# Optimization experiments

Measured on AMD Instinct MI355X. Metric: run time of the kernel, lower is better.

## Reference

```python
import jax, jax.numpy as jnp
import numpy as np

D_MODEL = 1024
NUM_HEADS = 16
D_HEAD = D_MODEL // NUM_HEADS
BATCH = 2
SEQ = 2048


def setup_inputs() -> dict:
    key = jax.random.key(0)
    ks = jax.random.split(key, 5)
    std = 0.02
    return {
        "x": jax.random.normal(ks[0], (BATCH, SEQ, D_MODEL), dtype=jnp.float32),
        "Wq": jax.random.normal(ks[1], (D_MODEL, D_MODEL), dtype=jnp.float32) * std,
        "Wk": jax.random.normal(ks[2], (D_MODEL, D_MODEL), dtype=jnp.float32) * std,
        "Wv": jax.random.normal(ks[3], (D_MODEL, D_MODEL), dtype=jnp.float32) * std,
        "Wo": jax.random.normal(ks[4], (D_MODEL, D_MODEL), dtype=jnp.float32) * std,
    }


def reference(x, Wq, Wk, Wv, Wo):
    batch, seq_len, d_model = x.shape
    h, dh = NUM_HEADS, D_HEAD

    def split_heads(W):
        # x @ W.T -> (b, s, d) -> (b, h, s, dh)
        p = jnp.einsum('bsd,ed->bse', x, W)
        return p.reshape(batch, seq_len, h, dh).transpose(0, 2, 1, 3)

    Q = split_heads(Wq)
    K = split_heads(Wk)
    V = split_heads(Wv)

    scale = 1.0 / jnp.sqrt(jnp.asarray(dh, dtype=x.dtype))
    scores = jnp.einsum('bhqd,bhkd->bhqk', Q, K) * scale
    causal = jnp.tril(jnp.ones((seq_len, seq_len), dtype=bool))
    scores = jnp.where(causal, scores, -jnp.inf)
    attn = jax.nn.softmax(scores, axis=-1)
    out = jnp.einsum('bhqk,bhkd->bhqd', attn, V)  # (b, h, s, dh)
    out = out.transpose(0, 2, 1, 3).reshape(batch, seq_len, d_model)
    return jnp.einsum('bsd,ed->bse', out, Wo)
```

## Files before the change

kernel.cpp:

```cpp
#include <hip/hip_runtime.h>

#define D_MODEL 1024
#define NUM_HEADS 16
#define D_HEAD 64
#define BATCH 2
#define SEQ 2048
#define MTOT (BATCH * SEQ)
#define PLANE ((size_t)MTOT * D_MODEL)
#define QSCALE 0.1803368801f

typedef unsigned short us;
typedef __bf16 bf16x8 __attribute__((ext_vector_type(8)));
typedef float floatx4 __attribute__((ext_vector_type(4)));

__device__ __forceinline__ unsigned int f2bf(float f) {
  union { float f; unsigned int i; } v; v.f = f;
  unsigned int r = v.i + 0x7FFFu + ((v.i >> 16) & 1u);
  return r >> 16;
}
__device__ __forceinline__ unsigned int f2bf_tr(float f) {
  union { float f; unsigned int i; } v; v.f = f;
  return v.i >> 16;
}

__global__ __launch_bounds__(256) void convert_all(const float* __restrict__ x,
                                                   const float* __restrict__ Wq,
                                                   const float* __restrict__ Wk,
                                                   const float* __restrict__ Wv,
                                                   const float* __restrict__ Wo,
                                                   us* __restrict__ xbf,
                                                   us* __restrict__ Wqkv,
                                                   us* __restrict__ Wobf) {
  const int i = blockIdx.x * 256 + threadIdx.x;
  const float* src;
  us* dst;
  if (i < (1 << 20)) {
    src = x + (size_t)i * 4;
    dst = xbf + (size_t)i * 4;
  } else {
    const int j = i - (1 << 20);
    const int w = j >> 18;
    const int o = j & ((1 << 18) - 1);
    if (w < 3) {
      const float* ws = (w == 0) ? Wq : (w == 1) ? Wk : Wv;
      src = ws + (size_t)o * 4;
      dst = Wqkv + (size_t)w * (D_MODEL * D_MODEL) + (size_t)o * 4;
    } else {
      src = Wo + (size_t)o * 4;
      dst = Wobf + (size_t)o * 4;
    }
  }
  float4 v = *(const float4*)src;
  uint2 pk;
  pk.x = f2bf(v.x) | (f2bf(v.y) << 16);
  pk.y = f2bf(v.z) | (f2bf(v.w) << 16);
  *(uint2*)dst = pk;
}

template <int CMODE>
__global__ __launch_bounds__(256) void gemm_mfma(const us* __restrict__ A,
                                                 const us* __restrict__ B,
                                                 void* __restrict__ Cv,
                                                 int M, int N, int K) {
  __shared__ __bf16 As[2][128 * 32];
  __shared__ __bf16 Bs[2][128 * 32];
  const int tid = threadIdx.x;
  const int wid = tid >> 6;
  const int lane = tid & 63;
  const int bm = blockIdx.y * 128;
  const int bn = blockIdx.x * 128;
  const int wm = (wid & 1) * 64;
  const int wn = (wid >> 1) * 64;
  const int lr = lane & 15;
  const int quad = lane >> 4;

  floatx4 acc[4][4] = {};
  const int cb0 = wid * 128;

  auto stage = [&](int buf, int k0) {
#pragma unroll
    for (int p = 0; p < 2; ++p) {
      const int cb = cb0 + p * 64;
      const int c = cb + lane;
      const us* ga = A + (size_t)(bm + (c >> 2)) * K + (k0 + (c & 3) * 8);
      const us* gb = B + (size_t)(bn + (c >> 2)) * K + (k0 + (c & 3) * 8);
      __builtin_amdgcn_global_load_lds((const __attribute__((address_space(1))) void*)ga,
                                       (__attribute__((address_space(3))) void*)(&As[buf][cb * 8]),
                                       16, 0, 0);
      __builtin_amdgcn_global_load_lds((const __attribute__((address_space(1))) void*)gb,
                                       (__attribute__((address_space(3))) void*)(&Bs[buf][cb * 8]),
                                       16, 0, 0);
    }
  };

  stage(0, 0);
  __syncthreads();

  int cur = 0;
  for (int k0 = 0; k0 < K; k0 += 32) {
    if (k0 + 32 < K) stage(cur ^ 1, k0 + 32);

    bf16x8 a[4], b[4];
#pragma unroll
    for (int i = 0; i < 4; ++i)
      a[i] = *(const bf16x8*)&As[cur][(wm + i * 16 + lr) * 32 + quad * 8];
#pragma unroll
    for (int j = 0; j < 4; ++j)
      b[j] = *(const bf16x8*)&Bs[cur][(wn + j * 16 + lr) * 32 + quad * 8];
#pragma unroll
    for (int i = 0; i < 4; ++i)
#pragma unroll
      for (int j = 0; j < 4; ++j)
        acc[i][j] = __builtin_amdgcn_mfma_f32_16x16x32_bf16(a[i], b[j], acc[i][j], 0, 0, 0);

    __syncthreads();
    cur ^= 1;
  }

#pragma unroll
  for (int i = 0; i < 4; ++i) {
#pragma unroll
    for (int j = 0; j < 4; ++j) {
      const int col = bn + wn + j * 16 + lr;
      if constexpr (CMODE == 1) {
        us* dst = (us*)Cv;
        const int plane = col >> 10;
        if (plane < 2) {
          const float s = (plane == 0) ? QSCALE : 1.0f;
#pragma unroll
          for (int r = 0; r < 4; ++r) {
            const int row = bm + wm + i * 16 + quad * 4 + r;
            dst[(size_t)plane * PLANE + (size_t)row * 1024 + (col & 1023)] =
                (us)f2bf(acc[i][j][r] * s);
          }
        } else {
          const int d = col & 63;
          const int hh = (col >> 6) & 15;
          const int row0 = bm + wm + i * 16 + quad * 4;
          const int bb = row0 >> 11;
          const int ss = row0 & 2047;
          uint2 pk;
          pk.x = f2bf(acc[i][j][0]) | (f2bf(acc[i][j][1]) << 16);
          pk.y = f2bf(acc[i][j][2]) | (f2bf(acc[i][j][3]) << 16);
          *(uint2*)&dst[2 * PLANE + ((size_t)((bb * 16 + hh) * 64 + d)) * 2048 + ss] = pk;
        }
      } else {
#pragma unroll
        for (int r = 0; r < 4; ++r) {
          const int row = bm + wm + i * 16 + quad * 4 + r;
          ((float*)Cv)[(size_t)row * N + col] = acc[i][j][r];
        }
      }
    }
  }
}

__global__ __launch_bounds__(256) void gemm_n64(const us* __restrict__ A,
                                                const us* __restrict__ B,
                                                float* __restrict__ C,
                                                int M, int N, int K) {
  __shared__ __bf16 As[2][128 * 32];
  __shared__ __bf16 Bs[2][64 * 32];
  const int tid = threadIdx.x;
  const int wid = tid >> 6;
  const int lane = tid & 63;
  const int bm = blockIdx.y * 128;
  const int bn = blockIdx.x * 64;
  const int wm = wid * 32;
  const int lr = lane & 15;
  const int quad = lane >> 4;

  floatx4 acc[2][4] = {};

  auto stage = [&](int buf, int k0) {
#pragma unroll
    for (int p = 0; p < 2; ++p) {
      const int cb = wid * 128 + p * 64;
      const int c = cb + lane;
      const us* ga = A + (size_t)(bm + (c >> 2)) * K + (k0 + (c & 3) * 8);
      __builtin_amdgcn_global_load_lds((const __attribute__((address_space(1))) void*)ga,
                                       (__attribute__((address_space(3))) void*)(&As[buf][cb * 8]),
                                       16, 0, 0);
    }
    const int cb2 = wid * 64;
    const int c2 = cb2 + lane;
    const us* gb = B + (size_t)(bn + (c2 >> 2)) * K + (k0 + (c2 & 3) * 8);
    __builtin_amdgcn_global_load_lds((const __attribute__((address_space(1))) void*)gb,
                                     (__attribute__((address_space(3))) void*)(&Bs[buf][cb2 * 8]),
                                     16, 0, 0);
  };

  stage(0, 0);
  __syncthreads();

  int cur = 0;
  for (int k0 = 0; k0 < K; k0 += 32) {
    if (k0 + 32 < K) stage(cur ^ 1, k0 + 32);

    bf16x8 a[2], b[4];
#pragma unroll
    for (int i = 0; i < 2; ++i)
      a[i] = *(const bf16x8*)&As[cur][(wm + i * 16 + lr) * 32 + quad * 8];
#pragma unroll
    for (int j = 0; j < 4; ++j)
      b[j] = *(const bf16x8*)&Bs[cur][(j * 16 + lr) * 32 + quad * 8];
#pragma unroll
    for (int i = 0; i < 2; ++i)
#pragma unroll
      for (int j = 0; j < 4; ++j)
        acc[i][j] = __builtin_amdgcn_mfma_f32_16x16x32_bf16(a[i], b[j], acc[i][j], 0, 0, 0);

    __syncthreads();
    cur ^= 1;
  }

#pragma unroll
  for (int i = 0; i < 2; ++i) {
#pragma unroll
    for (int j = 0; j < 4; ++j) {
      const int col = bn + j * 16 + lr;
#pragma unroll
      for (int r = 0; r < 4; ++r) {
        const int row = bm + wm + i * 16 + quad * 4 + r;
        C[(size_t)row * N + col] = acc[i][j][r];
      }
    }
  }
}

#define ASTR 72

__global__ __launch_bounds__(512, 2) void attn_mfma(const us* __restrict__ Qb,
                                                    const us* __restrict__ Kb,
                                                    const us* __restrict__ Vtg,
                                                    us* __restrict__ Ob) {
  const int bx = blockIdx.x;
  const int b = bx >> 8;
  const int idx = bx & 255;
  const int h = idx >> 4;
  const int s0 = idx & 15;
  const int strip = b ? (15 - s0) : s0;
  const int q0 = strip * 128;
  const int ntiles = 2 * strip + 2;
  const int tid = threadIdx.x;
  const int w = tid >> 6;
  const int lane = tid & 63;
  const int lr = lane & 15;
  const int quad = lane >> 4;

  __shared__ us Ks[2][64 * ASTR];
  __shared__ us Vs[2][64 * ASTR];
  __shared__ us Ps[8 * 16 * ASTR];

  const us* kbase = Kb + (size_t)(b * SEQ) * D_MODEL + h * D_HEAD;
  const us* vbase = Vtg + (size_t)((b * 16 + h) * 64) * 2048;
  us* const pg = &Ps[w * 16 * ASTR];

  const int grow = q0 + w * 16;
  const us* qp = Qb + (size_t)(b * SEQ + grow + lr) * D_MODEL + h * D_HEAD;
  const bf16x8 qa0 = *(const bf16x8*)(qp + quad * 8);
  const bf16x8 qa1 = *(const bf16x8*)(qp + 32 + quad * 8);

  floatx4 oacc[4] = {};
  floatx4 lacc = {};
  bf16x8 ones;
#pragma unroll
  for (int i = 0; i < 8; ++i) ones[i] = (__bf16)1.0f;

  const int srow = tid >> 3;
  const int schunk = tid & 7;

  uint4 kreg, vreg;
  kreg = *(const uint4*)(kbase + (size_t)srow * D_MODEL + schunk * 8);
  vreg = *(const uint4*)(vbase + (size_t)srow * 2048 + schunk * 8);
  *(uint4*)&Ks[0][srow * ASTR + schunk * 8] = kreg;
  *(uint4*)&Vs[0][srow * ASTR + schunk * 8] = vreg;
  __syncthreads();

  for (int t = 0; t < ntiles; ++t) {
    const int k0 = t * 64;
    const int cur = t & 1;
    const bool more = (t + 1 < ntiles);

    if (more) {
      const int kn = k0 + 64;
      kreg = *(const uint4*)(kbase + (size_t)(kn + srow) * D_MODEL + schunk * 8);
      vreg = *(const uint4*)(vbase + (size_t)srow * 2048 + kn + schunk * 8);
    }

#pragma unroll
    for (int jt = 0; jt < 4; ++jt) {
      const bf16x8 kb0 = *(const bf16x8*)&Ks[cur][(jt * 16 + lr) * ASTR + quad * 8];
      const bf16x8 kb1 = *(const bf16x8*)&Ks[cur][(jt * 16 + lr) * ASTR + 32 + quad * 8];
      floatx4 s = {};
      s = __builtin_amdgcn_mfma_f32_16x16x32_bf16(kb0, qa0, s, 0, 0, 0);
      s = __builtin_amdgcn_mfma_f32_16x16x32_bf16(kb1, qa1, s, 0, 0, 0);
      const int kb = k0 + jt * 16 + quad * 4;
      const bool needMask = (k0 + jt * 16 + 15 > grow);
      float p[4];
#pragma unroll
      for (int r = 0; r < 4; ++r) {
        float e = __builtin_amdgcn_exp2f(s[r]);
        if (needMask && (kb + r > grow + lr)) e = 0.f;
        p[r] = e;
      }
      uint2 pk;
      pk.x = f2bf_tr(p[0]) | (f2bf_tr(p[1]) << 16);
      pk.y = f2bf_tr(p[2]) | (f2bf_tr(p[3]) << 16);
      *(uint2*)&pg[lr * ASTR + jt * 16 + quad * 4] = pk;
    }

    const bf16x8 pa0 = *(const bf16x8*)&pg[lr * ASTR + quad * 8];
    const bf16x8 pa1 = *(const bf16x8*)&pg[lr * ASTR + 32 + quad * 8];
    lacc = __builtin_amdgcn_mfma_f32_16x16x32_bf16(ones, pa0, lacc, 0, 0, 0);
    lacc = __builtin_amdgcn_mfma_f32_16x16x32_bf16(ones, pa1, lacc, 0, 0, 0);
#pragma unroll
    for (int nt = 0; nt < 4; ++nt) {
      const bf16x8 vb0 = *(const bf16x8*)&Vs[cur][(nt * 16 + lr) * ASTR + quad * 8];
      const bf16x8 vb1 = *(const bf16x8*)&Vs[cur][(nt * 16 + lr) * ASTR + 32 + quad * 8];
      oacc[nt] = __builtin_amdgcn_mfma_f32_16x16x32_bf16(vb0, pa0, oacc[nt], 0, 0, 0);
      oacc[nt] = __builtin_amdgcn_mfma_f32_16x16x32_bf16(vb1, pa1, oacc[nt], 0, 0, 0);
    }

    if (more) {
      const int nxt = cur ^ 1;
      *(uint4*)&Ks[nxt][srow * ASTR + schunk * 8] = kreg;
      *(uint4*)&Vs[nxt][srow * ASTR + schunk * 8] = vreg;
    }
    __syncthreads();
  }

  const float inv = 1.f / lacc[0];
#pragma unroll
  for (int nt = 0; nt < 4; ++nt) {
    uint2 pk;
    pk.x = f2bf_tr(oacc[nt][0] * inv) | (f2bf_tr(oacc[nt][1] * inv) << 16);
    pk.y = f2bf_tr(oacc[nt][2] * inv) | (f2bf_tr(oacc[nt][3] * inv) << 16);
    *(uint2*)&pg[lr * ASTR + nt * 16 + quad * 4] = pk;
  }
#pragma unroll
  for (int p = 0; p < 2; ++p) {
    const int c = lane + 64 * p;
    *(uint4*)(Ob + (size_t)(b * SEQ + grow + (c >> 3)) * D_MODEL + h * D_HEAD + (c & 7) * 8) =
        *(const uint4*)&pg[(c >> 3) * ASTR + (c & 7) * 8];
  }
}

extern "C" void kernel_launch(void* const* d_in, const int* in_sizes, int n_in,
                              void* d_out, int out_size, void* d_ws, size_t ws_size,
                              hipStream_t stream) {
  const float* x  = (const float*)d_in[0];
  const float* Wq = (const float*)d_in[1];
  const float* Wk = (const float*)d_in[2];
  const float* Wv = (const float*)d_in[3];
  const float* Wo = (const float*)d_in[4];

  us* xbf = (us*)d_ws;
  us* Qb  = xbf + PLANE;
  us* Kb  = xbf + 2 * PLANE;
  us* Vt  = xbf + 3 * PLANE;
  us* Wobf = xbf + 4 * PLANE;
  us* Ab  = xbf;
  us* Wqkv = (us*)d_out;
  float* out = (float*)d_out;

  convert_all<<<8192, 256, 0, stream>>>(x, Wq, Wk, Wv, Wo, xbf, Wqkv, Wobf);

  gemm_mfma<1><<<dim3(3072 / 128, MTOT / 128), 256, 0, stream>>>(xbf, Wqkv, Qb, MTOT, 3072, D_MODEL);

  attn_mfma<<<512, 512, 0, stream>>>(Qb, Kb, Vt, Ab);

  gemm_n64<<<dim3(D_MODEL / 64, MTOT / 128), 256, 0, stream>>>(Ab, Wobf, out, MTOT, D_MODEL, D_MODEL);
}
```

Measured before the change: 174.7 us.

## Switch attention to 32x32x16 MFMA with 4 waves of 32 query rows

Rewrites the attention kernel so that each of 4 waves handles 32 query rows using 32x32x16 bf16 MFMA instead of 8 waves of 16 rows with 16x16x32. The block shrinks to 256 threads, and each thread now loads two K/V chunks per tile. The row-sum is accumulated in scalar registers and combined with a cross-half shuffle, replacing the extra MFMA against a ones vector. The aim is fewer MFMA issues and fewer LDS fragment reads per FLOP, at the cost of larger accumulators and higher register pressure.

```diff
diff --git a/kernel.cpp b/kernel.cpp
--- a/kernel.cpp
+++ b/kernel.cpp
@@ -12,6 +12,7 @@
 typedef unsigned short us;
 typedef __bf16 bf16x8 __attribute__((ext_vector_type(8)));
 typedef float floatx4 __attribute__((ext_vector_type(4)));
+typedef float floatx16 __attribute__((ext_vector_type(16)));
 
 __device__ __forceinline__ unsigned int f2bf(float f) {
   union { float f; unsigned int i; } v; v.f = f;
@@ -230,7 +231,7 @@
 
 #define ASTR 72
 
-__global__ __launch_bounds__(512, 2) void attn_mfma(const us* __restrict__ Qb,
+__global__ __launch_bounds__(256, 2) void attn_mfma(const us* __restrict__ Qb,
                                                     const us* __restrict__ Kb,
                                                     const us* __restrict__ Vtg,
                                                     us* __restrict__ Ob) {
@@ -245,36 +246,42 @@
   const int tid = threadIdx.x;
   const int w = tid >> 6;
   const int lane = tid & 63;
-  const int lr = lane & 15;
-  const int quad = lane >> 4;
+  const int l31 = lane & 31;
+  const int hi = lane >> 5;
 
   __shared__ us Ks[2][64 * ASTR];
   __shared__ us Vs[2][64 * ASTR];
-  __shared__ us Ps[8 * 16 * ASTR];
+  __shared__ us Ps[4 * 32 * ASTR];
 
   const us* kbase = Kb + (size_t)(b * SEQ) * D_MODEL + h * D_HEAD;
   const us* vbase = Vtg + (size_t)((b * 16 + h) * 64) * 2048;
-  us* const pg = &Ps[w * 16 * ASTR];
-
-  const int grow = q0 + w * 16;
-  const us* qp = Qb + (size_t)(b * SEQ + grow + lr) * D_MODEL + h * D_HEAD;
-  const bf16x8 qa0 = *(const bf16x8*)(qp + quad * 8);
-  const bf16x8 qa1 = *(const bf16x8*)(qp + 32 + quad * 8);
-
-  floatx4 oacc[4] = {};
-  floatx4 lacc = {};
-  bf16x8 ones;
-#pragma unroll
-  for (int i = 0; i < 8; ++i) ones[i] = (__bf16)1.0f;
-
-  const int srow = tid >> 3;
-  const int schunk = tid & 7;
-
-  uint4 kreg, vreg;
-  kreg = *(const uint4*)(kbase + (size_t)srow * D_MODEL + schunk * 8);
-  vreg = *(const uint4*)(vbase + (size_t)srow * 2048 + schunk * 8);
-  *(uint4*)&Ks[0][srow * ASTR + schunk * 8] = kreg;
-  *(uint4*)&Vs[0][srow * ASTR + schunk * 8] = vreg;
+  us* const pg = &Ps[w * 32 * ASTR];
+
+  const int grow = q0 + w * 32;
+  const int qrow = grow + l31;
+
+  const us* qp = Qb + (size_t)(b * SEQ + qrow) * D_MODEL + h * D_HEAD;
+  bf16x8 qa[4];
+#pragma unroll
+  for (int ks = 0; ks < 4; ++ks)
+    qa[ks] = *(const bf16x8*)(qp + ks * 16 + hi * 8);
+
+  floatx16 oacc[2] = {};
+  float lacc = 0.f;
+
+  uint4 kreg[2], vreg[2];
+#pragma unroll
+  for (int p = 0; p < 2; ++p) {
+    const int c = tid + 256 * p;
+    kreg[p] = *(const uint4*)(kbase + (size_t)(c >> 3) * D_MODEL + (c & 7) * 8);
+    vreg[p] = *(const uint4*)(vbase + (size_t)(c >> 3) * 2048 + (c & 7) * 8);
+  }
+#pragma unroll
+  for (int p = 0; p < 2; ++p) {
+    const int c = tid + 256 * p;
+    *(uint4*)&Ks[0][(c >> 3) * ASTR + (c & 7) * 8] = kreg[p];
+    *(uint4*)&Vs[0][(c >> 3) * ASTR + (c & 7) * 8] = vreg[p];
+  }
   __syncthreads();
 
   for (int t = 0; t < ntiles; ++t) {
@@ -284,62 +291,78 @@
 
     if (more) {
       const int kn = k0 + 64;
-      kreg = *(const uint4*)(kbase + (size_t)(kn + srow) * D_MODEL + schunk * 8);
-      vreg = *(const uint4*)(vbase + (size_t)srow * 2048 + kn + schunk * 8);
-    }
-
-#pragma unroll
-    for (int jt = 0; jt < 4; ++jt) {
-      const bf16x8 kb0 = *(const bf16x8*)&Ks[cur][(jt * 16 + lr) * ASTR + quad * 8];
-      const bf16x8 kb1 = *(const bf16x8*)&Ks[cur][(jt * 16 + lr) * ASTR + 32 + quad * 8];
-      floatx4 s = {};
-      s = __builtin_amdgcn_mfma_f32_16x16x32_bf16(kb0, qa0, s, 0, 0, 0);
-      s = __builtin_amdgcn_mfma_f32_16x16x32_bf16(kb1, qa1, s, 0, 0, 0);
-      const int kb = k0 + jt * 16 + quad * 4;
-      const bool needMask = (k0 + jt * 16 + 15 > grow);
-      float p[4];
-#pragma unroll
-      for (int r = 0; r < 4; ++r) {
-        float e = __builtin_amdgcn_exp2f(s[r]);
-        if (needMask && (kb + r > grow + lr)) e = 0.f;
-        p[r] = e;
-      }
-      uint2 pk;
-      pk.x = f2bf_tr(p[0]) | (f2bf_tr(p[1]) << 16);
-      pk.y = f2bf_tr(p[2]) | (f2bf_tr(p[3]) << 16);
-      *(uint2*)&pg[lr * ASTR + jt * 16 + quad * 4] = pk;
-    }
-
-    const bf16x8 pa0 = *(const bf16x8*)&pg[lr * ASTR + quad * 8];
-    const bf16x8 pa1 = *(const bf16x8*)&pg[lr * ASTR + 32 + quad * 8];
-    lacc = __builtin_amdgcn_mfma_f32_16x16x32_bf16(ones, pa0, lacc, 0, 0, 0);
-    lacc = __builtin_amdgcn_mfma_f32_16x16x32_bf16(ones, pa1, lacc, 0, 0, 0);
-#pragma unroll
-    for (int nt = 0; nt < 4; ++nt) {
-      const bf16x8 vb0 = *(const bf16x8*)&Vs[cur][(nt * 16 + lr) * ASTR + quad * 8];
-      const bf16x8 vb1 = *(const bf16x8*)&Vs[cur][(nt * 16 + lr) * ASTR + 32 + quad * 8];
-      oacc[nt] = __builtin_amdgcn_mfma_f32_16x16x32_bf16(vb0, pa0, oacc[nt], 0, 0, 0);
-      oacc[nt] = __builtin_amdgcn_mfma_f32_16x16x32_bf16(vb1, pa1, oacc[nt], 0, 0, 0);
-    }
+#pragma unroll
+      for (int p = 0; p < 2; ++p) {
+        const int c = tid + 256 * p;
+        kreg[p] = *(const uint4*)(kbase + (size_t)(kn + (c >> 3)) * D_MODEL + (c & 7) * 8);
+        vreg[p] = *(const uint4*)(vbase + (size_t)(c >> 3) * 2048 + kn + (c & 7) * 8);
+      }
+    }
+
+#pragma unroll
+    for (int kb = 0; kb < 2; ++kb) {
+      floatx16 s = {};
+#pragma unroll
+      for (int ks = 0; ks < 4; ++ks) {
+        const bf16x8 kf = *(const bf16x8*)&Ks[cur][(kb * 32 + l31) * ASTR + ks * 16 + hi * 8];
+        s = __builtin_amdgcn_mfma_f32_32x32x16_bf16(kf, qa[ks], s, 0, 0, 0);
+      }
+      const bool needMask = (k0 + kb * 32 + 31 > grow);
+      const int keyg = k0 + kb * 32 + 4 * hi;
+#pragma unroll
+      for (int g = 0; g < 4; ++g) {
+        float p[4];
+#pragma unroll
+        for (int r = 0; r < 4; ++r) {
+          float e = __builtin_amdgcn_exp2f(s[4 * g + r]);
+          if (needMask && (keyg + 8 * g + r > qrow)) e = 0.f;
+          p[r] = e;
+        }
+        lacc += (p[0] + p[1]) + (p[2] + p[3]);
+        uint2 pk;
+        pk.x = f2bf_tr(p[0]) | (f2bf_tr(p[1]) << 16);
+        pk.y = f2bf_tr(p[2]) | (f2bf_tr(p[3]) << 16);
+        *(uint2*)&pg[l31 * ASTR + kb * 32 + 8 * g + 4 * hi] = pk;
+      }
+    }
+
+    bf16x8 pf[4];
+#pragma unroll
+    for (int ks = 0; ks < 4; ++ks)
+      pf[ks] = *(const bf16x8*)&pg[l31 * ASTR + ks * 16 + hi * 8];
+#pragma unroll
+    for (int db = 0; db < 2; ++db)
+#pragma unroll
+      for (int ks = 0; ks < 4; ++ks) {
+        const bf16x8 vf = *(const bf16x8*)&Vs[cur][(db * 32 + l31) * ASTR + ks * 16 + hi * 8];
+        oacc[db] = __builtin_amdgcn_mfma_f32_32x32x16_bf16(vf, pf[ks], oacc[db], 0, 0, 0);
+      }
 
     if (more) {
       const int nxt = cur ^ 1;
-      *(uint4*)&Ks[nxt][srow * ASTR + schunk * 8] = kreg;
-      *(uint4*)&Vs[nxt][srow * ASTR + schunk * 8] = vreg;
+#pragma unroll
+      for (int p = 0; p < 2; ++p) {
+        const int c = tid + 256 * p;
+        *(uint4*)&Ks[nxt][(c >> 3) * ASTR + (c & 7) * 8] = kreg[p];
+        *(uint4*)&Vs[nxt][(c >> 3) * ASTR + (c & 7) * 8] = vreg[p];
+      }
     }
     __syncthreads();
   }
 
-  const float inv = 1.f / lacc[0];
-#pragma unroll
-  for (int nt = 0; nt < 4; ++nt) {
-    uint2 pk;
-    pk.x = f2bf_tr(oacc[nt][0] * inv) | (f2bf_tr(oacc[nt][1] * inv) << 16);
-    pk.y = f2bf_tr(oacc[nt][2] * inv) | (f2bf_tr(oacc[nt][3] * inv) << 16);
-    *(uint2*)&pg[lr * ASTR + nt * 16 + quad * 4] = pk;
-  }
-#pragma unroll
-  for (int p = 0; p < 2; ++p) {
+  const float ltot = lacc + __shfl(lacc, lane ^ 32, 64);
+  const float inv = 1.f / ltot;
+#pragma unroll
+  for (int db = 0; db < 2; ++db)
+#pragma unroll
+    for (int g = 0; g < 4; ++g) {
+      uint2 pk;
+      pk.x = f2bf_tr(oacc[db][4 * g + 0] * inv) | (f2bf_tr(oacc[db][4 * g + 1] * inv) << 16);
+      pk.y = f2bf_tr(oacc[db][4 * g + 2] * inv) | (f2bf_tr(oacc[db][4 * g + 3] * inv) << 16);
+      *(uint2*)&pg[l31 * ASTR + db * 32 + 8 * g + 4 * hi] = pk;
+    }
+#pragma unroll
+  for (int p = 0; p < 4; ++p) {
     const int c = lane + 64 * p;
     *(uint4*)(Ob + (size_t)(b * SEQ + grow + (c >> 3)) * D_MODEL + h * D_HEAD + (c & 7) * 8) =
         *(const uint4*)&pg[(c >> 3) * ASTR + (c & 7) * 8];
@@ -368,7 +391,7 @@
 
   gemm_mfma<1><<<dim3(3072 / 128, MTOT / 128), 256, 0, stream>>>(xbf, Wqkv, Qb, MTOT, 3072, D_MODEL);
 
-  attn_mfma<<<512, 512, 0, stream>>>(Qb, Kb, Vt, Ab);
+  attn_mfma<<<512, 256, 0, stream>>>(Qb, Kb, Vt, Ab);
 
   gemm_n64<<<dim3(D_MODEL / 64, MTOT / 128), 256, 0, stream>>>(Ab, Wobf, out, MTOT, D_MODEL, D_MODEL);
 }
```

New measurement: 204.2 us. +16.9%, slower.
